# Kernel tuning notes

Measured on AMD Instinct MI355X. Metric: run time of the kernel, lower is better.

The kernel has to match this reference:

```python
import jax, jax.numpy as jnp
import numpy as np

# Module constants (from init_kwargs)
M = 5          # frames per burst; query taken from frame M//2
WS = 8         # window_size
OW = 12        # overlap_wsize = int(WS*0.5) + WS
PAD = 2        # (OW - WS) // 2
NHEADS = 8
E = 64         # embed_dim
HD = E // NHEADS  # head_dim = 8


def setup_inputs() -> dict:
    key = jax.random.key(0)
    ks = jax.random.split(key, 9)
    B, H, W = 1, 128, 128
    return {
        "x": jax.random.normal(ks[0], (B * M, 3, H, W), jnp.float32),
        "w_high": jax.random.normal(ks[1], (E, 3), jnp.float32) * 0.1,
        "b_high": jnp.zeros((E,), jnp.float32),
        "gamma": jnp.ones((E,), jnp.float32),
        "beta": jnp.zeros((E,), jnp.float32),
        "w_qkv": jax.random.normal(ks[2], (3 * E, E), jnp.float32) * 0.05,
        "pos_q": jax.random.normal(ks[3], (WS * WS, E), jnp.float32) * 0.02,
        "pos_k": jax.random.normal(ks[4], (OW * OW, E), jnp.float32) * 0.02,
        "w_out": jax.random.normal(ks[5], (E, E), jnp.float32) * 0.05,
        "w_rgb": jax.random.normal(ks[6], (3, E), jnp.float32) * 0.1,
        "b_rgb": jnp.zeros((3,), jnp.float32),
    }


def _layernorm(x, g, b, eps=1e-6):
    mu = jnp.mean(x, axis=-1, keepdims=True)
    var = jnp.mean((x - mu) ** 2, axis=-1, keepdims=True)
    return (x - mu) * jax.lax.rsqrt(var + eps) * g + b


def _unfold_windows(t):
    # t: [BM, E, H, W] -> overlapping OWxOW windows, stride WS, pad PAD
    # returns [BM*n*n, OW*OW, E]  (matches torch Unfold + 'b (c j) i -> (b i) j c')
    BM, C, H, W = t.shape
    tp = jnp.pad(t, ((0, 0), (0, 0), (PAD, PAD), (PAD, PAD)))
    n = (H + 2 * PAD - OW) // WS + 1
    rows = jnp.arange(n)[:, None] * WS + jnp.arange(OW)[None, :]  # [n, OW]
    p = tp[:, :, rows, :]          # [BM, C, n, OW, Wp]
    p = p[:, :, :, :, rows]        # [BM, C, n, OW, n, OW]
    p = p.transpose(0, 2, 4, 3, 5, 1)  # [BM, n, n, OW, OW, C]
    return p.reshape(BM * n * n, OW * OW, C)


def reference(x, w_high, b_high, gamma, beta, w_qkv, pos_q, pos_k, w_out, w_rgb, b_rgb):
    BM, _, H, W = x.shape
    B = BM // M
    # 1x1 conv 3 -> E
    feat = jnp.einsum('bchw,ec->behw', x, w_high) + b_high[None, :, None, None]
    # layernorm over channels (as sequence [BM, HW, E])
    xs = feat.reshape(BM, E, H * W).transpose(0, 2, 1)
    xs = _layernorm(xs, gamma, beta)
    # qkv projection (no bias)
    qkv = (xs @ w_qkv.T).reshape(BM, H, W, 3, E)
    Q = qkv[..., 0, :].transpose(0, 3, 1, 2)  # [BM, E, H, W]
    K = qkv[..., 1, :].transpose(0, 3, 1, 2)
    V = qkv[..., 2, :].transpose(0, 3, 1, 2)
    # broadcast the middle-frame query across all M frames
    Qb = Q.reshape(B, M, E, H, W)
    Q = jnp.broadcast_to(Qb[:, M // 2:M // 2 + 1], (B, M, E, H, W)).reshape(BM, E, H, W)
    nH, nW = H // WS, W // WS
    # non-overlapping query windows
    Qw = Q.reshape(BM, E, nH, WS, nW, WS).transpose(0, 2, 4, 3, 5, 1).reshape(-1, WS * WS, E)
    # overlapping key/value halo windows
    Kw = _unfold_windows(K)
    Vw = _unfold_windows(V)
    Qw = Qw + pos_q
    Kw = Kw + pos_k
    s = Qw.shape[0]
    q = Qw.reshape(s, WS * WS, NHEADS, HD)
    k = Kw.reshape(s, OW * OW, NHEADS, HD)
    v = Vw.reshape(s, OW * OW, NHEADS, HD)
    # attention with flash-attn default scale head_dim**-0.5
    att = jnp.einsum('sqhd,skhd->shqk', q, k) * (HD ** -0.5)
    att = jax.nn.softmax(att, axis=-1)
    out = jnp.einsum('shqk,skhd->sqhd', att, v)  # [s, WS*WS, NHEADS, HD]
    # '(b nh nw) (ph pw) h d -> b (nh ph nw pw) (h d)'
    out = out.reshape(BM, nH, nW, WS, WS, E).transpose(0, 1, 3, 2, 4, 5).reshape(BM, H * W, E)
    out = out @ w_out.T
    mixed = out.reshape(BM, H, W, E).transpose(0, 3, 1, 2) + feat
    rgb = jnp.einsum('behw,ce->bchw', mixed, w_rgb) + b_rgb[None, :, None, None]
    return rgb.reshape(B, -1, H, W)
```

## Files before the change

### kernel.cpp

```cpp
#include <hip/hip_runtime.h>
#include <hip/hip_bf16.h>

#define HW 16384
#define W_IMG 128
#define BM_TOT 5
#define PRE 0.5101179482f

typedef __attribute__((ext_vector_type(8))) short bf16x8;
typedef __attribute__((ext_vector_type(4))) float f32x4;

__device__ __forceinline__ short f2b(float f) {
    __hip_bfloat16 h = __float2bfloat16(f);
    union { __hip_bfloat16 h; short s; } c; c.h = h; return c.s;
}
__device__ __forceinline__ float b2f(short s) {
    union { unsigned u; float f; } v; v.u = ((unsigned)(unsigned short)s) << 16;
    return v.f;
}
__device__ __forceinline__ unsigned pk2(float a, float b) {
    __hip_bfloat162 h = __float22bfloat162_rn(make_float2(a, b));
    union { __hip_bfloat162 h; unsigned u; } c; c.h = h; return c.u;
}
__device__ __forceinline__ float fexp2(float x) {
#if __has_builtin(__builtin_amdgcn_exp2f)
    return __builtin_amdgcn_exp2f(x);
#else
    float r; asm("v_exp_f32 %0, %1" : "=v"(r) : "v"(x)); return r;
#endif
}

__global__ __launch_bounds__(256) void k_qkv(
    const float* __restrict__ x, const float* __restrict__ w_qkv,
    const float* __restrict__ w_high, const float* __restrict__ b_high,
    const float* __restrict__ gamma, const float* __restrict__ beta,
    const float* __restrict__ pos_q, const float* __restrict__ w_rgb,
    const float* __restrict__ w_out,
    float* __restrict__ featrgb, short* __restrict__ qmid,
    short* __restrict__ kbuf, short* __restrict__ vbuf,
    short* __restrict__ wcombb)
{
    __shared__ char smem[39680];
    short* XS  = (short*)smem;
    short* TLk = (short*)(smem + 9216);
    short* TLv = (short*)(smem + 18432);
    short* TLq = (short*)(smem + 27648);
    float* WL  = (float*)(smem + 36864);
    float* WRL = (float*)(smem + 36864 + 2048);

    const int tid = threadIdx.x, blk = blockIdx.x;
    const int bm = blk >> 8, p0 = (blk & 255) * 64;
    const int pixbase = blk * 64;
    const int wv = tid >> 6, lane = tid & 63;
    const int col = lane & 15, grp = lane >> 4;

    if (tid < 64) {
        WL[tid * 8 + 0] = w_high[tid * 3];
        WL[tid * 8 + 1] = w_high[tid * 3 + 1];
        WL[tid * 8 + 2] = w_high[tid * 3 + 2];
        WL[tid * 8 + 3] = b_high[tid];
        WL[tid * 8 + 4] = gamma[tid];
        WL[tid * 8 + 5] = beta[tid];
    } else if (tid < 112) {
        ((float4*)WRL)[tid - 64] = ((const float4*)w_rgb)[tid - 64];
    }
    __syncthreads();

    {
        const int px_l = tid >> 2, part = tid & 3;
        const int p = p0 + px_l;
        const float* xp = x + (size_t)bm * 3 * HW + p;
        const float x0 = xp[0], x1 = xp[HW], x2 = xp[2 * HW];
        float f[16]; float s = 0.f, s2 = 0.f;
        #pragma unroll
        for (int j = 0; j < 16; ++j) {
            const int ch = part * 16 + j;
            float4 wa = *(const float4*)&WL[ch * 8];
            f[j] = fmaf(wa.x, x0, fmaf(wa.y, x1, fmaf(wa.z, x2, wa.w)));
            s += f[j]; s2 = fmaf(f[j], f[j], s2);
        }
        float r0 = 0.f, r1 = 0.f, r2 = 0.f;
        #pragma unroll
        for (int j = 0; j < 16; ++j) {
            const float fj = f[j];
            r0 = fmaf(fj, WRL[part * 16 + j], r0);
            r1 = fmaf(fj, WRL[64 + part * 16 + j], r1);
            r2 = fmaf(fj, WRL[128 + part * 16 + j], r2);
        }
        s  += __shfl_xor(s, 1);  s  += __shfl_xor(s, 2);
        s2 += __shfl_xor(s2, 1); s2 += __shfl_xor(s2, 2);
        r0 += __shfl_xor(r0, 1); r0 += __shfl_xor(r0, 2);
        r1 += __shfl_xor(r1, 1); r1 += __shfl_xor(r1, 2);
        r2 += __shfl_xor(r2, 1); r2 += __shfl_xor(r2, 2);
        if (part < 3) {
            float rv = part == 0 ? r0 : (part == 1 ? r1 : r2);
            featrgb[((size_t)bm * 3 + part) * HW + p] = rv;
        }
        const float mu = s * 0.015625f;
        const float var = s2 * 0.015625f - mu * mu;
        const float rs = rsqrtf(var + 1e-6f);
        unsigned xw[8];
        #pragma unroll
        for (int j2 = 0; j2 < 8; ++j2) {
            const int ch = part * 16 + 2 * j2;
            float4 g0 = *(const float4*)&WL[ch * 8 + 4];
            float4 g1 = *(const float4*)&WL[ch * 8 + 12];
            xw[j2] = pk2((f[2 * j2] - mu) * rs * g0.x + g0.y,
                         (f[2 * j2 + 1] - mu) * rs * g1.x + g1.y);
        }
        *(uint4*)&XS[px_l * 72 + part * 16]     = make_uint4(xw[0], xw[1], xw[2], xw[3]);
        *(uint4*)&XS[px_l * 72 + part * 16 + 8] = make_uint4(xw[4], xw[5], xw[6], xw[7]);
    }

    bf16x8 Bf[3][2];
    #pragma unroll
    for (int jj = 0; jj < 3; ++jj) {
        int jt = wv + jj * 4;
        #pragma unroll
        for (int kc = 0; kc < 2; ++kc) {
            const float* src = &w_qkv[(jt * 16 + col) * 64 + kc * 32 + grp * 8];
            union { bf16x8 v; unsigned u[4]; } tmp;
            #pragma unroll
            for (int i = 0; i < 4; ++i) tmp.u[i] = pk2(src[2 * i], src[2 * i + 1]);
            Bf[jj][kc] = tmp.v;
        }
    }
    __syncthreads();

    #pragma unroll
    for (int pt = 0; pt < 4; ++pt) {
        bf16x8 A0 = *(const bf16x8*)&XS[(pt * 16 + col) * 72 + grp * 8];
        bf16x8 A1 = *(const bf16x8*)&XS[(pt * 16 + col) * 72 + 32 + grp * 8];

        f32x4 aK = {0.f, 0.f, 0.f, 0.f};
        aK = __builtin_amdgcn_mfma_f32_16x16x32_bf16(Bf[1][0], A0, aK, 0, 0, 0);
        aK = __builtin_amdgcn_mfma_f32_16x16x32_bf16(Bf[1][1], A1, aK, 0, 0, 0);
        uint2 kw = {pk2(aK[0], aK[1]), pk2(aK[2], aK[3])};
        *(uint2*)&TLk[(pt * 16 + col) * 72 + wv * 16 + grp * 4] = kw;

        f32x4 aV = {0.f, 0.f, 0.f, 0.f};
        aV = __builtin_amdgcn_mfma_f32_16x16x32_bf16(A0, Bf[2][0], aV, 0, 0, 0);
        aV = __builtin_amdgcn_mfma_f32_16x16x32_bf16(A1, Bf[2][1], aV, 0, 0, 0);
        #pragma unroll
        for (int i = 0; i < 4; ++i)
            TLv[(pt * 16 + grp * 4 + i) * 72 + wv * 16 + col] = f2b(aV[i]);

        if (bm == 2) {
            f32x4 aQ = {0.f, 0.f, 0.f, 0.f};
            aQ = __builtin_amdgcn_mfma_f32_16x16x32_bf16(Bf[0][0], A0, aQ, 0, 0, 0);
            aQ = __builtin_amdgcn_mfma_f32_16x16x32_bf16(Bf[0][1], A1, aQ, 0, 0, 0);
            int p = p0 + pt * 16 + col;
            int qq = ((p >> 7) & 7) * 8 + (p & 7);
            float4 pq = *(const float4*)&pos_q[qq * 64 + wv * 16 + grp * 4];
            uint2 qw = {pk2((aQ[0] + pq.x) * PRE, (aQ[1] + pq.y) * PRE),
                        pk2((aQ[2] + pq.z) * PRE, (aQ[3] + pq.w) * PRE)};
            *(uint2*)&TLq[(pt * 16 + col) * 72 + wv * 16 + grp * 4] = qw;
        }
    }
    __syncthreads();

    #pragma unroll
    for (int it = 0; it < 2; ++it) {
        int j = it * 256 + tid;
        int row = j >> 3, seg = j & 7;
        *(uint4*)&kbuf[((size_t)pixbase + row) * 64 + seg * 8] =
            *(const uint4*)&TLk[row * 72 + seg * 8];
        *(uint4*)&vbuf[((size_t)pixbase + row) * 64 + seg * 8] =
            *(const uint4*)&TLv[row * 72 + seg * 8];
        if (bm == 2)
            *(uint4*)&qmid[((size_t)p0 + row) * 64 + seg * 8] =
                *(const uint4*)&TLq[row * 72 + seg * 8];
    }

    if (blk == 0) {
        float* WOL = (float*)TLk;
        __syncthreads();
        for (int i = tid; i < 4096; i += 256) WOL[i] = w_out[i];
        __syncthreads();
        for (int i = tid; i < 1024; i += 256) {
            short wc = 0;
            if (i < 192) {
                int c = i >> 6, e = i & 63;
                float a = 0.f;
                #pragma unroll 8
                for (int e2 = 0; e2 < 64; ++e2)
                    a = fmaf(WRL[c * 64 + e2], WOL[e2 * 64 + e], a);
                wc = f2b(a);
            }
            wcombb[i] = wc;
        }
    }
}

__global__ __launch_bounds__(512, 6) void k_attn(
    const short* __restrict__ qmid, const short* __restrict__ kbuf,
    const short* __restrict__ vbuf,
    const float* __restrict__ pos_k, const float* __restrict__ b_rgb,
    const float* __restrict__ featrgb, const short* __restrict__ wcombb,
    float* __restrict__ outp)
{
    __shared__ char smem[48448];
    short* Klds = (short*)smem;
    short* Vt   = (short*)(smem + 20736);
    short* OL   = (short*)smem;

    const int tid = threadIdx.x, blk = blockIdx.x;
    const int bm = blk >> 8, widx = blk & 255;
    const int wi = widx >> 4, wj = widx & 15;
    const int head = tid >> 6, lane = tid & 63;
    const int col = lane & 15, grp = lane >> 4;

    for (int idx = tid; idx < 1152; idx += 512) {
        int kk = idx >> 3, chunk = idx & 7;
        int r = kk / 12, c = kk - r * 12;
        int hh = wi * 8 - 2 + r, ww = wj * 8 - 2 + c;
        uint4 kraw = {0, 0, 0, 0};
        if ((unsigned)hh < 128u && (unsigned)ww < 128u)
            kraw = *(const uint4*)&kbuf[((size_t)bm * HW + hh * W_IMG + ww) * 64 + chunk * 8];
        const float* pk = &pos_k[kk * 64 + chunk * 8];
        float4 pk0 = *(const float4*)pk;
        float4 pk1 = *(const float4*)(pk + 4);
        union { uint4 q; short s[8]; } ku; ku.q = kraw;
        uint4 ko;
        ko.x = pk2(b2f(ku.s[0]) + pk0.x, b2f(ku.s[1]) + pk0.y);
        ko.y = pk2(b2f(ku.s[2]) + pk0.z, b2f(ku.s[3]) + pk0.w);
        ko.z = pk2(b2f(ku.s[4]) + pk1.x, b2f(ku.s[5]) + pk1.y);
        ko.w = pk2(b2f(ku.s[6]) + pk1.z, b2f(ku.s[7]) + pk1.w);
        *(uint4*)&Klds[kk * 72 + chunk * 8] = ko;
    }

    for (int idx = tid; idx < 1152; idx += 512) {
        int chunk = idx / 144, kk = idx - chunk * 144;
        int r = kk / 12, c = kk - r * 12;
        int hh = wi * 8 - 2 + r, ww = wj * 8 - 2 + c;
        uint4 vraw = {0, 0, 0, 0};
        if ((unsigned)hh < 128u && (unsigned)ww < 128u)
            vraw = *(const uint4*)&vbuf[((size_t)bm * HW + hh * W_IMG + ww) * 64 + chunk * 8];
        union { uint4 q; short s[8]; } vu; vu.q = vraw;
        #pragma unroll
        for (int cc = 0; cc < 8; ++cc)
            Vt[(chunk * 8 + cc) * 152 + kk] = vu.s[cc];
    }
    if (tid < 64) *(uint4*)&Vt[tid * 152 + 144] = (uint4){0, 0, 0, 0};
    if (tid < 2)  *(uint4*)&Vt[64 * 152 + tid * 8] = (uint4){0, 0, 0, 0};

    uint4 qraw[4] = {{0,0,0,0},{0,0,0,0},{0,0,0,0},{0,0,0,0}};
    if (grp == 0) {
        #pragma unroll
        for (int qt = 0; qt < 4; ++qt) {
            int q = qt * 16 + col;
            int pix = (wi * 8 + (q >> 3)) * W_IMG + wj * 8 + (q & 7);
            qraw[qt] = *(const uint4*)&qmid[(size_t)pix * 64 + head * 8];
        }
    }
    __syncthreads();

    unsigned* PBh = (unsigned*)(smem + 40224 + head * 1024);
    const int slot_w = (grp * 16 + (col ^ grp)) * 4;
    const int g0 = 2 * (grp & 1);
    const int slotr1 = (g0 * 16 + (col ^ g0)) * 4 + (grp >> 1) * 2;
    const int slotr2 = ((g0 + 1) * 16 + (col ^ (g0 + 1))) * 4 + (grp >> 1) * 2;

    f32x4 oacc[4];
    float linv[4];

    #pragma unroll
    for (int qt = 0; qt < 4; ++qt) {
        union { bf16x8 v; uint4 r; } qu; qu.r = qraw[qt];
        const bf16x8 qf = qu.v;

        float l = 0.f;
        unsigned pw[20];
        __builtin_amdgcn_s_setprio(1);
        #pragma unroll
        for (int t = 0; t < 9; ++t) {
            bf16x8 kf = *(const bf16x8*)&Klds[(t * 16 + col) * 72 + head * 8];
            f32x4 sct = __builtin_amdgcn_mfma_f32_16x16x32_bf16(
                kf, qf, (f32x4){0.f, 0.f, 0.f, 0.f}, 0, 0, 0);
            float e0 = fexp2(sct[0]), e1 = fexp2(sct[1]);
            float e2 = fexp2(sct[2]), e3 = fexp2(sct[3]);
            l += (e0 + e1) + (e2 + e3);
            pw[2 * t]     = pk2(e0, e1);
            pw[2 * t + 1] = pk2(e2, e3);
        }
        __builtin_amdgcn_s_setprio(0);
        pw[18] = 0u; pw[19] = 0u;
        l += __shfl_xor(l, 16);
        l += __shfl_xor(l, 32);
        linv[qt] = __builtin_amdgcn_rcpf(l);

        *(uint4*)(PBh + slot_w) = make_uint4(pw[0], pw[1], pw[2], pw[3]);
        f32x4 oa = {0.f, 0.f, 0.f, 0.f};
        __builtin_amdgcn_s_setprio(1);
        #pragma unroll
        for (int kt2 = 0; kt2 < 5; ++kt2) {
            uint2 r1 = *(const uint2*)(PBh + slotr1);
            uint2 r2 = *(const uint2*)(PBh + slotr2);
            if (kt2 < 4)
                *(uint4*)(PBh + slot_w) =
                    make_uint4(pw[4 * kt2 + 4], pw[4 * kt2 + 5], pw[4 * kt2 + 6], pw[4 * kt2 + 7]);
            union { bf16x8 v; unsigned u[4]; } pf;
            pf.u[0] = r1.x; pf.u[1] = r1.y; pf.u[2] = r2.x; pf.u[3] = r2.y;
            bf16x8 vf = *(const bf16x8*)&Vt[(head * 8 + (lane & 7)) * 152 + kt2 * 32 + grp * 8];
            oa = __builtin_amdgcn_mfma_f32_16x16x32_bf16(vf, pf.v, oa, 0, 0, 0);
        }
        __builtin_amdgcn_s_setprio(0);
        oacc[qt] = oa;
    }
    __syncthreads();

    if (grp < 2) {
        #pragma unroll
        for (int qt = 0; qt < 4; ++qt) {
            float s = linv[qt];
            uint2 ow;
            ow.x = pk2(oacc[qt][0] * s, oacc[qt][1] * s);
            ow.y = pk2(oacc[qt][2] * s, oacc[qt][3] * s);
            *(uint2*)&OL[(qt * 16 + col) * 72 + head * 8 + grp * 4] = ow;
        }
    }
    __syncthreads();

    if (head < 4) {
        const int qt = head;
        f32x4 acc = {0.f, 0.f, 0.f, 0.f};
        #pragma unroll
        for (int kc = 0; kc < 2; ++kc) {
            bf16x8 ao = *(const bf16x8*)&OL[(qt * 16 + col) * 72 + kc * 32 + grp * 8];
            bf16x8 bo = *(const bf16x8*)&wcombb[col * 64 + kc * 32 + grp * 8];
            acc = __builtin_amdgcn_mfma_f32_16x16x32_bf16(ao, bo, acc, 0, 0, 0);
        }
        if (col < 3) {
            float br = b_rgb[col];
            const float* frp = featrgb + ((size_t)bm * 3 + col) * HW;
            #pragma unroll
            for (int i = 0; i < 4; ++i) {
                int qs = qt * 16 + grp * 4 + i;
                int pix = (wi * 8 + (qs >> 3)) * W_IMG + wj * 8 + (qs & 7);
                outp[(size_t)bm * 3 * HW + col * HW + pix] = acc[i] + frp[pix] + br;
            }
        }
    }
}

extern "C" void kernel_launch(void* const* d_in, const int* in_sizes, int n_in,
                              void* d_out, int out_size, void* d_ws, size_t ws_size,
                              hipStream_t stream) {
    const float* x      = (const float*)d_in[0];
    const float* w_high = (const float*)d_in[1];
    const float* b_high = (const float*)d_in[2];
    const float* gamma  = (const float*)d_in[3];
    const float* beta   = (const float*)d_in[4];
    const float* w_qkv  = (const float*)d_in[5];
    const float* pos_q  = (const float*)d_in[6];
    const float* pos_k  = (const float*)d_in[7];
    const float* w_out  = (const float*)d_in[8];
    const float* w_rgb  = (const float*)d_in[9];
    const float* b_rgb  = (const float*)d_in[10];
    float* out = (float*)d_out;

    float* featrgb = (float*)d_ws;
    short* kbuf    = (short*)(featrgb + (size_t)BM_TOT * 3 * HW);
    short* vbuf    = kbuf + (size_t)BM_TOT * HW * 64;
    short* qmid    = vbuf + (size_t)BM_TOT * HW * 64;
    short* wcombb  = qmid + (size_t)HW * 64;

    k_qkv<<<BM_TOT * 256, 256, 0, stream>>>(x, w_qkv, w_high, b_high, gamma, beta,
                                            pos_q, w_rgb, w_out,
                                            featrgb, qmid, kbuf, vbuf, wcombb);
    k_attn<<<BM_TOT * 256, 512, 0, stream>>>(qmid, kbuf, vbuf, pos_k,
                                             b_rgb, featrgb, wcombb, out);
}
```

Before: 55.35 us.

## Stage K/V per head in each wave and drop block barriers in attention

```diff
diff --git a/kernel.cpp b/kernel.cpp
--- a/kernel.cpp
+++ b/kernel.cpp
@@ -53,6 +53,11 @@
     const int wv = tid >> 6, lane = tid & 63;
     const int col = lane & 15, grp = lane >> 4;
 
+    const int px_l = tid >> 2, part = tid & 3;
+    const int p_glob = p0 + px_l;
+    const float* xp = x + (size_t)bm * 3 * HW + p_glob;
+    const float x0 = xp[0], x1 = xp[HW], x2 = xp[2 * HW];
+
     if (tid < 64) {
         WL[tid * 8 + 0] = w_high[tid * 3];
         WL[tid * 8 + 1] = w_high[tid * 3 + 1];
@@ -66,10 +71,6 @@
     __syncthreads();
 
     {
-        const int px_l = tid >> 2, part = tid & 3;
-        const int p = p0 + px_l;
-        const float* xp = x + (size_t)bm * 3 * HW + p;
-        const float x0 = xp[0], x1 = xp[HW], x2 = xp[2 * HW];
         float f[16]; float s = 0.f, s2 = 0.f;
         #pragma unroll
         for (int j = 0; j < 16; ++j) {
@@ -93,7 +94,7 @@
         r2 += __shfl_xor(r2, 1); r2 += __shfl_xor(r2, 2);
         if (part < 3) {
             float rv = part == 0 ? r0 : (part == 1 ? r1 : r2);
-            featrgb[((size_t)bm * 3 + part) * HW + p] = rv;
+            featrgb[((size_t)bm * 3 + part) * HW + p_glob] = rv;
         }
         const float mu = s * 0.015625f;
         const float var = s2 * 0.015625f - mu * mu;
@@ -117,10 +118,11 @@
         int jt = wv + jj * 4;
         #pragma unroll
         for (int kc = 0; kc < 2; ++kc) {
-            const float* src = &w_qkv[(jt * 16 + col) * 64 + kc * 32 + grp * 8];
+            const float4* src = (const float4*)&w_qkv[(jt * 16 + col) * 64 + kc * 32 + grp * 8];
+            float4 a = src[0], b = src[1];
             union { bf16x8 v; unsigned u[4]; } tmp;
-            #pragma unroll
-            for (int i = 0; i < 4; ++i) tmp.u[i] = pk2(src[2 * i], src[2 * i + 1]);
+            tmp.u[0] = pk2(a.x, a.y); tmp.u[1] = pk2(a.z, a.w);
+            tmp.u[2] = pk2(b.x, b.y); tmp.u[3] = pk2(b.z, b.w);
             Bf[jj][kc] = tmp.v;
         }
     }
@@ -209,50 +211,45 @@
     const int head = tid >> 6, lane = tid & 63;
     const int col = lane & 15, grp = lane >> 4;
 
-    for (int idx = tid; idx < 1152; idx += 512) {
-        int kk = idx >> 3, chunk = idx & 7;
-        int r = kk / 12, c = kk - r * 12;
-        int hh = wi * 8 - 2 + r, ww = wj * 8 - 2 + c;
-        uint4 kraw = {0, 0, 0, 0};
-        if ((unsigned)hh < 128u && (unsigned)ww < 128u)
-            kraw = *(const uint4*)&kbuf[((size_t)bm * HW + hh * W_IMG + ww) * 64 + chunk * 8];
-        const float* pk = &pos_k[kk * 64 + chunk * 8];
+    uint4 qraw[4] = {{0,0,0,0},{0,0,0,0},{0,0,0,0},{0,0,0,0}};
+    if (grp == 0) {
+        #pragma unroll
+        for (int qt = 0; qt < 4; ++qt) {
+            int q = qt * 16 + col;
+            int pix = (wi * 8 + (q >> 3)) * W_IMG + wj * 8 + (q & 7);
+            qraw[qt] = *(const uint4*)&qmid[(size_t)pix * 64 + head * 8];
+        }
+    }
+
+    #pragma unroll
+    for (int i = 0; i < 3; ++i) {
+        const int kk = lane + i * 64;
+        if (i == 2 && lane >= 16) continue;
+        const int r = kk / 12, c = kk - r * 12;
+        const int hh = wi * 8 - 2 + r, ww = wj * 8 - 2 + c;
+        uint4 kraw = {0, 0, 0, 0}, vraw = {0, 0, 0, 0};
+        if ((unsigned)hh < 128u && (unsigned)ww < 128u) {
+            size_t off = ((size_t)bm * HW + hh * W_IMG + ww) * 64 + head * 8;
+            kraw = *(const uint4*)&kbuf[off];
+            vraw = *(const uint4*)&vbuf[off];
+        }
+        const float* pk = &pos_k[kk * 64 + head * 8];
         float4 pk0 = *(const float4*)pk;
         float4 pk1 = *(const float4*)(pk + 4);
-        union { uint4 q; short s[8]; } ku; ku.q = kraw;
+        union { uint4 q; short s[8]; } ku, vu;
+        ku.q = kraw; vu.q = vraw;
         uint4 ko;
         ko.x = pk2(b2f(ku.s[0]) + pk0.x, b2f(ku.s[1]) + pk0.y);
         ko.y = pk2(b2f(ku.s[2]) + pk0.z, b2f(ku.s[3]) + pk0.w);
         ko.z = pk2(b2f(ku.s[4]) + pk1.x, b2f(ku.s[5]) + pk1.y);
         ko.w = pk2(b2f(ku.s[6]) + pk1.z, b2f(ku.s[7]) + pk1.w);
-        *(uint4*)&Klds[kk * 72 + chunk * 8] = ko;
-    }
-
-    for (int idx = tid; idx < 1152; idx += 512) {
-        int chunk = idx / 144, kk = idx - chunk * 144;
-        int r = kk / 12, c = kk - r * 12;
-        int hh = wi * 8 - 2 + r, ww = wj * 8 - 2 + c;
-        uint4 vraw = {0, 0, 0, 0};
-        if ((unsigned)hh < 128u && (unsigned)ww < 128u)
-            vraw = *(const uint4*)&vbuf[((size_t)bm * HW + hh * W_IMG + ww) * 64 + chunk * 8];
-        union { uint4 q; short s[8]; } vu; vu.q = vraw;
+        *(uint4*)&Klds[kk * 72 + head * 8] = ko;
         #pragma unroll
         for (int cc = 0; cc < 8; ++cc)
-            Vt[(chunk * 8 + cc) * 152 + kk] = vu.s[cc];
-    }
-    if (tid < 64) *(uint4*)&Vt[tid * 152 + 144] = (uint4){0, 0, 0, 0};
-    if (tid < 2)  *(uint4*)&Vt[64 * 152 + tid * 8] = (uint4){0, 0, 0, 0};
-
-    uint4 qraw[4] = {{0,0,0,0},{0,0,0,0},{0,0,0,0},{0,0,0,0}};
-    if (grp == 0) {
-        #pragma unroll
-        for (int qt = 0; qt < 4; ++qt) {
-            int q = qt * 16 + col;
-            int pix = (wi * 8 + (q >> 3)) * W_IMG + wj * 8 + (q & 7);
-            qraw[qt] = *(const uint4*)&qmid[(size_t)pix * 64 + head * 8];
-        }
-    }
-    __syncthreads();
+            Vt[(head * 8 + cc) * 152 + kk] = vu.s[cc];
+    }
+    if (lane < 8) *(uint4*)&Vt[(head * 8 + lane) * 152 + 144] = (uint4){0, 0, 0, 0};
+    if (head == 7 && lane == 0) *(uint4*)&Vt[64 * 152] = (uint4){0, 0, 0, 0};
 
     unsigned* PBh = (unsigned*)(smem + 40224 + head * 1024);
     const int slot_w = (grp * 16 + (col ^ grp)) * 4;
@@ -306,7 +303,6 @@
         __builtin_amdgcn_s_setprio(0);
         oacc[qt] = oa;
     }
-    __syncthreads();
 
     if (grp < 2) {
         #pragma unroll
```

Result: no change. 54.85 us (-0.9%).
